# Performance work log

Measured on AMD Instinct MI355X. Metric: run time of the kernel, lower is better.

The kernel has to match this reference:

```python
import jax, jax.numpy as jnp
import numpy as np

N_NODES = 100000
N_EDGES = 1600000
D_IN = 256
D_OUT = 128


def setup_inputs() -> dict:
    key = jax.random.key(0)
    k1, k2, k3, k4, k5 = jax.random.split(key, 5)
    features = jax.random.normal(k1, (N_NODES, D_IN), dtype=jnp.float32)
    # Xavier-uniform init for weight [in, out]
    limit = float(np.sqrt(6.0 / (D_IN + D_OUT)))
    weight = jax.random.uniform(k2, (D_IN, D_OUT), dtype=jnp.float32, minval=-limit, maxval=limit)
    edge_rows = jax.random.randint(k3, (N_EDGES,), 0, N_NODES, dtype=jnp.int32)
    edge_cols = jax.random.randint(k4, (N_EDGES,), 0, N_NODES, dtype=jnp.int32)
    edge_vals = jax.random.uniform(k5, (N_EDGES,), dtype=jnp.float32)
    return {
        "features": features,
        "weight": weight,
        "edge_rows": edge_rows,
        "edge_cols": edge_cols,
        "edge_vals": edge_vals,
    }


def reference(features, weight, edge_rows, edge_cols, edge_vals):
    # support = X @ W : [N, D_OUT]
    support = features @ weight
    # SpMM with COO adjacency: out[i] = sum_{e: row[e]==i} vals[e] * support[col[e]]
    gathered = edge_vals[:, None] * support[edge_cols]        # [E, D_OUT]
    output = jax.ops.segment_sum(gathered, edge_rows, num_segments=N_NODES)
    # active=True -> fused ReLU
    return jax.nn.relu(output)
```

## Files before the change

kernel.cpp:

```cpp
#include <hip/hip_runtime.h>

#define N_NODES 100000
#define N_EDGES 1600000
#define D_IN    256
#define D_OUT   128

__global__ __launch_bounds__(128) void gcn_gemm_kernel(
    const float* __restrict__ X,
    const float* __restrict__ W,
    float* __restrict__ support)
{
    __shared__ float xs[32][D_IN];

    const int tid = threadIdx.x;
    const int c = tid & 31;
    const int r = tid >> 5;
    const int node0 = blockIdx.x * 32;

    {
        const float4* X4 = (const float4*)(X + (size_t)node0 * D_IN);
        float4* xs4 = (float4*)&xs[0][0];
#pragma unroll
        for (int i = 0; i < 16; ++i) {
            int L = i * 128 + tid;
            xs4[L] = X4[L];
        }
    }
    __syncthreads();

    const float4* W4 = (const float4*)W;
    float4 acc[8];
#pragma unroll
    for (int i = 0; i < 8; ++i) acc[i] = make_float4(0.f, 0.f, 0.f, 0.f);

#pragma unroll 4
    for (int k = 0; k < D_IN; ++k) {
        const float4 w = W4[k * 32 + c];
#pragma unroll
        for (int rr = 0; rr < 8; ++rr) {
            const float xv = xs[r * 8 + rr][k];
            acc[rr].x = fmaf(xv, w.x, acc[rr].x);
            acc[rr].y = fmaf(xv, w.y, acc[rr].y);
            acc[rr].z = fmaf(xv, w.z, acc[rr].z);
            acc[rr].w = fmaf(xv, w.w, acc[rr].w);
        }
    }

    float4* S4 = (float4*)support;
#pragma unroll
    for (int rr = 0; rr < 8; ++rr)
        S4[(size_t)(node0 + r * 8 + rr) * 32 + c] = acc[rr];
}

__global__ __launch_bounds__(256) void gcn_hist_kernel(
    const int* __restrict__ rows, int* __restrict__ counts)
{
    int e = blockIdx.x * 256 + threadIdx.x;
    if (e < N_EDGES) atomicAdd(&counts[rows[e]], 1);
}

__global__ __launch_bounds__(256) void gcn_scan1_kernel(
    const int* __restrict__ counts, int* __restrict__ off, int* __restrict__ bsums)
{
    __shared__ int t[256];
    const int tid = threadIdx.x;
    const int i0 = blockIdx.x * 1024 + tid * 4;

    int c0 = 0, c1 = 0, c2 = 0, c3 = 0;
    if (i0 + 3 < N_NODES) {
        int4 v = *(const int4*)&counts[i0];
        c0 = v.x; c1 = v.y; c2 = v.z; c3 = v.w;
    } else {
        if (i0 + 0 < N_NODES) c0 = counts[i0 + 0];
        if (i0 + 1 < N_NODES) c1 = counts[i0 + 1];
        if (i0 + 2 < N_NODES) c2 = counts[i0 + 2];
        if (i0 + 3 < N_NODES) c3 = counts[i0 + 3];
    }
    const int s = c0 + c1 + c2 + c3;
    t[tid] = s;
    __syncthreads();

    for (int d = 1; d < 256; d <<= 1) {
        int x = t[tid];
        int add = (tid >= d) ? t[tid - d] : 0;
        __syncthreads();
        t[tid] = x + add;
        __syncthreads();
    }
    const int excl = t[tid] - s;
    if (tid == 255) bsums[blockIdx.x] = t[255];

    const int e0 = excl;
    const int e1 = e0 + c0;
    const int e2 = e1 + c1;
    const int e3 = e2 + c2;
    if (i0 + 0 < N_NODES) off[i0 + 0] = e0;
    if (i0 + 1 < N_NODES) off[i0 + 1] = e1;
    if (i0 + 2 < N_NODES) off[i0 + 2] = e2;
    if (i0 + 3 < N_NODES) off[i0 + 3] = e3;
}

__global__ __launch_bounds__(128) void gcn_scan2_kernel(int* __restrict__ bsums, int nb)
{
    __shared__ int t[128];
    const int tid = threadIdx.x;
    const int v = (tid < nb) ? bsums[tid] : 0;
    t[tid] = v;
    __syncthreads();
    for (int d = 1; d < 128; d <<= 1) {
        int x = t[tid];
        int add = (tid >= d) ? t[tid - d] : 0;
        __syncthreads();
        t[tid] = x + add;
        __syncthreads();
    }
    if (tid < nb) bsums[tid] = t[tid] - v;
}

__global__ __launch_bounds__(256) void gcn_scan3_kernel(
    const int* __restrict__ bsums, int* __restrict__ off, int* __restrict__ cursor)
{
    int i = blockIdx.x * 256 + threadIdx.x;
    if (i < N_NODES) {
        int o = off[i] + bsums[i >> 10];
        off[i] = o;
        cursor[i] = o;
    }
}

__global__ __launch_bounds__(256) void gcn_scatter_kernel(
    const int* __restrict__ rows, const int* __restrict__ cols,
    const float* __restrict__ vals, int* __restrict__ cursor,
    int2* __restrict__ edges)
{
    int e = blockIdx.x * 256 + threadIdx.x;
    if (e < N_EDGES) {
        int pos = atomicAdd(&cursor[rows[e]], 1);
        edges[pos] = make_int2(cols[e], __float_as_int(vals[e]));
    }
}

__global__ __launch_bounds__(256) void gcn_aggregate_kernel(
    const int* __restrict__ off, const int* __restrict__ ends,
    const int2* __restrict__ edges, const float* __restrict__ support,
    float* __restrict__ out)
{
    const int node = blockIdx.x * 4 + (threadIdx.x >> 6);
    if (node >= N_NODES) return;
    const int lane = threadIdx.x & 63;

    const int start = off[node];
    const int end   = ends[node];

    const float2* S2 = (const float2*)support;
    float2 acc = make_float2(0.f, 0.f);

    for (int base = start; base < end; base += 64) {
        int m = end - base;
        if (m > 64) m = 64;
        int2 e = edges[base + (lane < m ? lane : 0)];
        for (int j = 0; j < m; ++j) {
            const int   col = __shfl(e.x, j);
            const float v   = __int_as_float(__shfl(e.y, j));
            const float2 s  = S2[(size_t)col * 64 + lane];
            acc.x = fmaf(v, s.x, acc.x);
            acc.y = fmaf(v, s.y, acc.y);
        }
    }

    float2 o;
    o.x = acc.x > 0.f ? acc.x : 0.f;
    o.y = acc.y > 0.f ? acc.y : 0.f;
    ((float2*)out)[(size_t)node * 64 + lane] = o;
}

extern "C" void kernel_launch(void* const* d_in, const int* in_sizes, int n_in,
                              void* d_out, int out_size, void* d_ws, size_t ws_size,
                              hipStream_t stream)
{
    const float* X    = (const float*)d_in[0];
    const float* W    = (const float*)d_in[1];
    const int*   rows = (const int*)  d_in[2];
    const int*   cols = (const int*)  d_in[3];
    const float* vals = (const float*)d_in[4];
    float* out = (float*)d_out;

    char* ws = (char*)d_ws;
    size_t p = 0;
    float* support = (float*)(ws + p); p += (size_t)N_NODES * D_OUT * 4;
    int*   counts  = (int*)  (ws + p); p += (size_t)N_NODES * 4;
    int*   off     = (int*)  (ws + p); p += (size_t)N_NODES * 4;
    int*   cursor  = (int*)  (ws + p); p += (size_t)N_NODES * 4;
    int*   bsums   = (int*)  (ws + p); p += 512;
    int2*  edges   = (int2*) (ws + p); p += (size_t)N_EDGES * 8;
    (void)ws_size;

    const int NB = (N_NODES + 1023) / 1024;

    gcn_gemm_kernel<<<N_NODES / 32, 128, 0, stream>>>(X, W, support);

    hipMemsetAsync(counts, 0, (size_t)N_NODES * 4, stream);
    gcn_hist_kernel<<<(N_EDGES + 255) / 256, 256, 0, stream>>>(rows, counts);
    gcn_scan1_kernel<<<NB, 256, 0, stream>>>(counts, off, bsums);
    gcn_scan2_kernel<<<1, 128, 0, stream>>>(bsums, NB);
    gcn_scan3_kernel<<<(N_NODES + 255) / 256, 256, 0, stream>>>(bsums, off, cursor);
    gcn_scatter_kernel<<<(N_EDGES + 255) / 256, 256, 0, stream>>>(rows, cols, vals, cursor, edges);

    gcn_aggregate_kernel<<<(N_NODES + 3) / 4, 256, 0, stream>>>(
        off, cursor, edges, support, out);
}
```

Before: 579.4 us.

## Use bf16 MFMA for dense GEMM and store support matrix in bf16

```diff
diff --git a/kernel.cpp b/kernel.cpp
--- a/kernel.cpp
+++ b/kernel.cpp
@@ -5,51 +5,97 @@
 #define D_IN    256
 #define D_OUT   128
 
-__global__ __launch_bounds__(128) void gcn_gemm_kernel(
+typedef __attribute__((ext_vector_type(8))) short short8;
+typedef __attribute__((ext_vector_type(4))) float floatx4;
+
+static __device__ __forceinline__ ushort f2bf(float f) {
+    union { float f; unsigned u; } v; v.f = f;
+    unsigned r = v.u + 0x7fffu + ((v.u >> 16) & 1u);
+    return (ushort)(r >> 16);
+}
+
+__global__ __launch_bounds__(256) void gcn_gemm_mfma(
     const float* __restrict__ X,
     const float* __restrict__ W,
-    float* __restrict__ support)
-{
-    __shared__ float xs[32][D_IN];
-
-    const int tid = threadIdx.x;
-    const int c = tid & 31;
-    const int r = tid >> 5;
-    const int node0 = blockIdx.x * 32;
-
-    {
-        const float4* X4 = (const float4*)(X + (size_t)node0 * D_IN);
-        float4* xs4 = (float4*)&xs[0][0];
-#pragma unroll
-        for (int i = 0; i < 16; ++i) {
-            int L = i * 128 + tid;
-            xs4[L] = X4[L];
+    ushort* __restrict__ supp)
+{
+    __shared__ ushort wp[32 * 128 * 8];
+
+    const int tid  = threadIdx.x;
+    const int lane = tid & 63;
+    const int wid  = tid >> 6;
+    const int node0 = blockIdx.x * 128;
+
+#pragma unroll
+    for (int i = 0; i < 16; ++i) {
+        const int p   = i * 256 + tid;
+        const int kg  = p >> 7;
+        const int col = p & 127;
+        const float* wsrc = W + (size_t)(kg * 8) * D_OUT + col;
+        short8 v;
+#pragma unroll
+        for (int ki = 0; ki < 8; ++ki)
+            v[ki] = (short)f2bf(wsrc[(size_t)ki * D_OUT]);
+        *(short8*)&wp[(size_t)p * 8] = v;
+    }
+    __syncthreads();
+
+    const int r0    = node0 + wid * 32;
+    const int g     = lane >> 4;
+    const int arow0 = r0 + (lane & 15);
+    const int arow1 = arow0 + 16;
+    const int crow0 = arow0 < N_NODES - 1 ? arow0 : N_NODES - 1;
+    const int crow1 = arow1 < N_NODES - 1 ? arow1 : N_NODES - 1;
+
+    const float* xp0 = X + (size_t)crow0 * D_IN + g * 8;
+    const float* xp1 = X + (size_t)crow1 * D_IN + g * 8;
+
+    floatx4 acc[2][8];
+#pragma unroll
+    for (int t = 0; t < 2; ++t)
+#pragma unroll
+        for (int n = 0; n < 8; ++n)
+            acc[t][n] = (floatx4){0.f, 0.f, 0.f, 0.f};
+
+#pragma unroll
+    for (int ks = 0; ks < 8; ++ks) {
+        const float4 u0 = *(const float4*)(xp0 + ks * 32);
+        const float4 u1 = *(const float4*)(xp0 + ks * 32 + 4);
+        const float4 u2 = *(const float4*)(xp1 + ks * 32);
+        const float4 u3 = *(const float4*)(xp1 + ks * 32 + 4);
+        short8 a0, a1;
+        a0[0] = (short)f2bf(u0.x); a0[1] = (short)f2bf(u0.y);
+        a0[2] = (short)f2bf(u0.z); a0[3] = (short)f2bf(u0.w);
+        a0[4] = (short)f2bf(u1.x); a0[5] = (short)f2bf(u1.y);
+        a0[6] = (short)f2bf(u1.z); a0[7] = (short)f2bf(u1.w);
+        a1[0] = (short)f2bf(u2.x); a1[1] = (short)f2bf(u2.y);
+        a1[2] = (short)f2bf(u2.z); a1[3] = (short)f2bf(u2.w);
+        a1[4] = (short)f2bf(u3.x); a1[5] = (short)f2bf(u3.y);
+        a1[6] = (short)f2bf(u3.z); a1[7] = (short)f2bf(u3.w);
+
+        const int kg = ks * 4 + g;
+#pragma unroll
+        for (int n = 0; n < 8; ++n) {
+            const short8 b = *(const short8*)&wp[(size_t)((kg << 7) + n * 16 + (lane & 15)) * 8];
+            acc[0][n] = __builtin_amdgcn_mfma_f32_16x16x32_bf16(a0, b, acc[0][n], 0, 0, 0);
+            acc[1][n] = __builtin_amdgcn_mfma_f32_16x16x32_bf16(a1, b, acc[1][n], 0, 0, 0);
         }
     }
-    __syncthreads();
-
-    const float4* W4 = (const float4*)W;
-    float4 acc[8];
-#pragma unroll
-    for (int i = 0; i < 8; ++i) acc[i] = make_float4(0.f, 0.f, 0.f, 0.f);
-
-#pragma unroll 4
-    for (int k = 0; k < D_IN; ++k) {
-        const float4 w = W4[k * 32 + c];
-#pragma unroll
-        for (int rr = 0; rr < 8; ++rr) {
-            const float xv = xs[r * 8 + rr][k];
-            acc[rr].x = fmaf(xv, w.x, acc[rr].x);
-            acc[rr].y = fmaf(xv, w.y, acc[rr].y);
-            acc[rr].z = fmaf(xv, w.z, acc[rr].z);
-            acc[rr].w = fmaf(xv, w.w, acc[rr].w);
+
+#pragma unroll
+    for (int t = 0; t < 2; ++t) {
+        const int rbase = r0 + t * 16 + (lane >> 4) * 4;
+#pragma unroll
+        for (int n = 0; n < 8; ++n) {
+            const int col = n * 16 + (lane & 15);
+#pragma unroll
+            for (int i = 0; i < 4; ++i) {
+                const int row = rbase + i;
+                if (row < N_NODES)
+                    supp[(size_t)row * D_OUT + col] = f2bf(acc[t][n][i]);
+            }
         }
     }
-
-    float4* S4 = (float4*)support;
-#pragma unroll
-    for (int rr = 0; rr < 8; ++rr)
-        S4[(size_t)(node0 + r * 8 + rr) * 32 + c] = acc[rr];
 }
 
 __global__ __launch_bounds__(256) void gcn_hist_kernel(
@@ -142,7 +188,7 @@
 
 __global__ __launch_bounds__(256) void gcn_aggregate_kernel(
     const int* __restrict__ off, const int* __restrict__ ends,
-    const int2* __restrict__ edges, const float* __restrict__ support,
+    const int2* __restrict__ edges, const unsigned* __restrict__ supp2,
     float* __restrict__ out)
 {
     const int node = blockIdx.x * 4 + (threadIdx.x >> 6);
@@ -152,25 +198,24 @@
     const int start = off[node];
     const int end   = ends[node];
 
-    const float2* S2 = (const float2*)support;
-    float2 acc = make_float2(0.f, 0.f);
+    float accx = 0.f, accy = 0.f;
 
     for (int base = start; base < end; base += 64) {
         int m = end - base;
         if (m > 64) m = 64;
         int2 e = edges[base + (lane < m ? lane : 0)];
         for (int j = 0; j < m; ++j) {
-            const int   col = __shfl(e.x, j);
-            const float v   = __int_as_float(__shfl(e.y, j));
-            const float2 s  = S2[(size_t)col * 64 + lane];
-            acc.x = fmaf(v, s.x, acc.x);
-            acc.y = fmaf(v, s.y, acc.y);
+            const int      col = __shfl(e.x, j);
+            const float    v   = __int_as_float(__shfl(e.y, j));
+            const unsigned s   = supp2[(size_t)col * 64 + lane];
+            accx = fmaf(v, __uint_as_float(s << 16), accx);
+            accy = fmaf(v, __uint_as_float(s & 0xffff0000u), accy);
         }
     }
 
     float2 o;
-    o.x = acc.x > 0.f ? acc.x : 0.f;
-    o.y = acc.y > 0.f ? acc.y : 0.f;
+    o.x = accx > 0.f ? accx : 0.f;
+    o.y = accy > 0.f ? accy : 0.f;
     ((float2*)out)[(size_t)node * 64 + lane] = o;
 }
 
@@ -187,19 +232,19 @@
 
     char* ws = (char*)d_ws;
     size_t p = 0;
-    float* support = (float*)(ws + p); p += (size_t)N_NODES * D_OUT * 4;
-    int*   counts  = (int*)  (ws + p); p += (size_t)N_NODES * 4;
-    int*   off     = (int*)  (ws + p); p += (size_t)N_NODES * 4;
-    int*   cursor  = (int*)  (ws + p); p += (size_t)N_NODES * 4;
-    int*   bsums   = (int*)  (ws + p); p += 512;
-    int2*  edges   = (int2*) (ws + p); p += (size_t)N_EDGES * 8;
+    ushort* supp   = (ushort*)(ws + p); p += (size_t)N_NODES * D_OUT * 2;
+    int*    counts = (int*)   (ws + p); p += (size_t)N_NODES * 4;
+    int*    off    = (int*)   (ws + p); p += (size_t)N_NODES * 4;
+    int*    cursor = (int*)   (ws + p); p += (size_t)N_NODES * 4;
+    int*    bsums  = (int*)   (ws + p); p += 512;
+    int2*   edges  = (int2*)  (ws + p); p += (size_t)N_EDGES * 8;
     (void)ws_size;
 
     const int NB = (N_NODES + 1023) / 1024;
 
-    gcn_gemm_kernel<<<N_NODES / 32, 128, 0, stream>>>(X, W, support);
-
-    hipMemsetAsync(counts, 0, (size_t)N_NODES * 4, stream);
+    gcn_gemm_mfma<<<(N_NODES + 127) / 128, 256, 0, stream>>>(X, W, supp);
+
+    (void)hipMemsetAsync(counts, 0, (size_t)N_NODES * 4, stream);
     gcn_hist_kernel<<<(N_EDGES + 255) / 256, 256, 0, stream>>>(rows, counts);
     gcn_scan1_kernel<<<NB, 256, 0, stream>>>(counts, off, bsums);
     gcn_scan2_kernel<<<1, 128, 0, stream>>>(bsums, NB);
@@ -207,5 +252,5 @@
     gcn_scatter_kernel<<<(N_EDGES + 255) / 256, 256, 0, stream>>>(rows, cols, vals, cursor, edges);
 
     gcn_aggregate_kernel<<<(N_NODES + 3) / 4, 256, 0, stream>>>(
-        off, cursor, edges, support, out);
-}
+        off, cursor, edges, (const unsigned*)supp, out);
+}
```

Result: faster. 480.4 us (-17.1%).
